# Kernel tuning notes

Hardware: AMD Instinct MI355X
Metric: run time of the kernel (lower is better)

Reference implementation:

```python
import jax, jax.numpy as jnp
import numpy as np

B, DIM, H, W = 8, 512, 32, 32
HC, WC = 32, 32
NH, DH = 8, 64
DE = NH * DH  # dim_embed = 512


def setup_inputs() -> dict:
    key = jax.random.key(0)
    ks = jax.random.split(key, 6)
    return {
        "x": jax.random.normal(ks[0], (B, DIM, H, W), jnp.float32),
        "context": jax.random.normal(ks[1], (B, DIM, HC, WC), jnp.float32),
        "gamma": jnp.ones((DIM, 1, 1), jnp.float32),
        "w_q": jax.random.normal(ks[2], (DE, DIM), jnp.float32) * 0.02,
        "w_k": jax.random.normal(ks[3], (DE, DIM), jnp.float32) * 0.02,
        "w_v": jax.random.normal(ks[4], (DE, DIM), jnp.float32) * 0.02,
        "w_proj": jax.random.normal(ks[5], (DIM, DE), jnp.float32) * 0.02,
    }


def _rms_norm(t, gamma, scale):
    # torch F.normalize(dim=1): x / max(||x||_2, 1e-12) along channel axis
    nrm = jnp.sqrt(jnp.sum(t * t, axis=1, keepdims=True))
    return t / jnp.maximum(nrm, 1e-12) * scale * gamma


def _split_heads(t, h, w):
    # 'b (c n) h w -> (b n) (h w) c' with c=DH, n=NH
    b = t.shape[0]
    t = t.reshape(b, DH, NH, h, w).transpose(0, 2, 3, 4, 1)  # b n h w c
    return t.reshape(b * NH, h * w, DH)


def reference(x, context, gamma, w_q, w_k, w_v, w_proj):
    scale = float(DIM) ** 0.5
    xn = _rms_norm(x, gamma, scale)
    # faithful to source bug: self.norm (not norm_context) applied to context
    cn = _rms_norm(context, gamma, scale)

    q = jnp.einsum('bchw,oc->bohw', xn, w_q)
    k = jnp.einsum('bchw,oc->bohw', cn, w_k)
    v = jnp.einsum('bchw,oc->bohw', cn, w_v)

    q = _split_heads(q, H, W)      # (B*NH, H*W, DH)
    k = _split_heads(k, HC, WC)    # (B*NH, HC*WC, DH)
    v = _split_heads(v, HC, WC)

    qk = jnp.einsum('bmc,bnc->bmn', q, k) * (float(DH) ** -0.5)
    attn = jnp.einsum('bmn,bnc->bmc', jax.nn.softmax(qk, axis=-1) + 1e-8, v) + 1e-8

    # '(b n) (h w) c -> b (c n) h w'
    attn = attn.reshape(B, NH, H, W, DH).transpose(0, 4, 1, 2, 3).reshape(B, DE, H, W)
    return jnp.einsum('bchw,oc->bohw', attn, w_proj)
```

## Files before the change

### kernel.cpp

```cpp
#include <hip/hip_runtime.h>
#include <hip/hip_bf16.h>


typedef _Float16 half8v __attribute__((ext_vector_type(8)));
typedef __attribute__((ext_vector_type(4))) float float4v;

__device__ inline ushort f2h(float f) {
  union { _Float16 h; ushort u; } cv;
  cv.h = (_Float16)f;
  return cv.u;
}

__device__ inline void stage16(const void* g, void* l) {
  __builtin_amdgcn_global_load_lds(
      (const __attribute__((address_space(1))) unsigned*)g,
      (__attribute__((address_space(3))) unsigned*)l, 16, 0, 0);
}

__global__ __launch_bounds__(256) void tq_kernel(
    const float* __restrict__ x, const float* __restrict__ ctx,
    ushort* __restrict__ xT, ushort* __restrict__ cT,
    float* __restrict__ sx, float* __restrict__ sc) {
  const int tensor = blockIdx.z;
  const int b = blockIdx.y;
  const int pos0 = blockIdx.x << 5;
  const float* src = tensor ? ctx : x;
  ushort* dstT = tensor ? cT : xT;
  float* dstS = tensor ? sc : sx;
  const int t = threadIdx.x;

  __shared__ ushort tile[32 * 512];
  __shared__ float part[32][32];
  unsigned* tile32 = (unsigned*)tile;

  const int pcq = t & 7;
  const int crg = t >> 3;
  float ssq[4] = {0.f, 0.f, 0.f, 0.f};

  const float* srcb = src + ((size_t)b * 512) * 1024 + pos0;
  for (int p = 0; p < 8; ++p) {
    const int cr0 = p * 64 + crg * 2;
    float4 v0 = *(const float4*)&srcb[(size_t)cr0 * 1024 + pcq * 4];
    float4 v1 = *(const float4*)&srcb[(size_t)(cr0 + 1) * 1024 + pcq * 4];
    ssq[0] += v0.x * v0.x + v1.x * v1.x;
    ssq[1] += v0.y * v0.y + v1.y * v1.y;
    ssq[2] += v0.z * v0.z + v1.z * v1.z;
    ssq[3] += v0.w * v0.w + v1.w * v1.w;
    const int cp = cr0 >> 1;
    float e0[4] = {v0.x, v0.y, v0.z, v0.w};
    float e1[4] = {v1.x, v1.y, v1.z, v1.w};
#pragma unroll
    for (int j = 0; j < 4; ++j) {
      const int posl = pcq * 4 + j;
      unsigned pk = (unsigned)f2h(e0[j]) | ((unsigned)f2h(e1[j]) << 16);
      tile32[posl * 256 + (cp ^ posl)] = pk;
    }
  }
#pragma unroll
  for (int j = 0; j < 4; ++j) part[crg][pcq * 4 + j] = ssq[j];
  __syncthreads();
  if (t < 32) {
    float s = 0.f;
#pragma unroll
    for (int g2 = 0; g2 < 32; ++g2) s += part[g2][t];
    dstS[b * 1024 + pos0 + t] = 22.627416997969522f / fmaxf(sqrtf(s), 1e-12f);
  }
  ushort* ob = dstT + ((size_t)b * 1024 + pos0) * 512;
#pragma unroll
  for (int ii = 0; ii < 8; ++ii) {
    const int m = t + ii * 256;
    const int posl = m >> 6, c16 = m & 63;
    uint4 u;
    u.x = tile32[posl * 256 + ((c16 * 4 + 0) ^ posl)];
    u.y = tile32[posl * 256 + ((c16 * 4 + 1) ^ posl)];
    u.z = tile32[posl * 256 + ((c16 * 4 + 2) ^ posl)];
    u.w = tile32[posl * 256 + ((c16 * 4 + 3) ^ posl)];
    *(uint4*)&ob[(size_t)posl * 512 + c16 * 8] = u;
  }
}

__global__ __launch_bounds__(256) void wconv_kernel(
    const float* __restrict__ wq, const float* __restrict__ wk,
    const float* __restrict__ wv, const float* __restrict__ wp,
    const float* __restrict__ gamma, ushort* __restrict__ wf) {
  const int m = blockIdx.y;
  const float* W = (m == 0) ? wq : (m == 1) ? wk : (m == 2) ? wv : wp;
  const int r = blockIdx.x * 4 + (threadIdx.x >> 6);
  const int c8 = (threadIdx.x & 63) * 8;
  ushort h[8];
  if (m < 3) {
    const int o = ((r & 63) << 3) + (r >> 6);
    const float* wr_ = &W[(size_t)o * 512 + c8];
#pragma unroll
    for (int j = 0; j < 8; ++j) h[j] = f2h(wr_[j] * gamma[c8 + j]);
  } else {
#pragma unroll
    for (int j = 0; j < 8; ++j) {
      const int cc = c8 + j;
      const int cs = ((cc & 63) << 3) + (cc >> 6);
      h[j] = f2h(W[(size_t)r * 512 + cs]);
    }
  }
  ushort* dst = &wf[((size_t)m * 512 + r) * 512 + c8];
  uint4 u;
  u.x = (unsigned)h[0] | ((unsigned)h[1] << 16);
  u.y = (unsigned)h[2] | ((unsigned)h[3] << 16);
  u.z = (unsigned)h[4] | ((unsigned)h[5] << 16);
  u.w = (unsigned)h[6] | ((unsigned)h[7] << 16);
  *(uint4*)dst = u;
}

__global__ __launch_bounds__(256, 2) void qkv_kernel(
    const ushort* __restrict__ xT, const ushort* __restrict__ cT,
    const ushort* __restrict__ wf, const float* __restrict__ sx,
    const float* __restrict__ sc, ushort* __restrict__ qh,
    ushort* __restrict__ kh, ushort* __restrict__ vt) {
  const int z = blockIdx.z;
  const int proj = z % 3;
  const int b = z / 3;
  const ushort* XT = (proj == 0) ? xT : cT;
  const float* S = (proj == 0) ? sx : sc;
  const ushort* WF = wf + (size_t)proj * 262144;
  const int pos0 = blockIdx.x << 7;
  const int o0 = blockIdx.y << 7;

  __shared__ __align__(16) unsigned char lds[65536];
  unsigned char* Al = lds;
  unsigned char* Bl = lds + 32768;

  const int t = threadIdx.x, w = t >> 6, lane = t & 63;
  const int g = lane >> 4, l15 = lane & 15;
  const int wr = w >> 1, wc = w & 1;
  const int srow_ = lane >> 3;
  const int sslot16 = ((lane & 7) ^ srow_) << 4;

  const unsigned char* Asrc =
      (const unsigned char*)(XT + ((size_t)b * 1024 + pos0) * 512);
  const unsigned char* Bsrc = (const unsigned char*)(WF + (size_t)o0 * 512);

#define QSTAGE(buf, kk)                                                     \
  do {                                                                      \
    _Pragma("unroll") for (int i = 0; i < 4; ++i) {                         \
      const int j = (w << 2) + i;                                           \
      stage16(Asrc + (size_t)((j << 3) + srow_) * 1024 + (kk)*128 + sslot16,\
              Al + (buf)*16384 + (j << 10));                                \
      stage16(Bsrc + (size_t)((j << 3) + srow_) * 1024 + (kk)*128 + sslot16,\
              Bl + (buf)*16384 + (j << 10));                                \
    }                                                                       \
  } while (0)

  float4v acc[4][4];
#pragma unroll
  for (int i = 0; i < 4; ++i)
#pragma unroll
    for (int j2 = 0; j2 < 4; ++j2) acc[i][j2] = (float4v){0.f, 0.f, 0.f, 0.f};

  QSTAGE(0, 0);
  __syncthreads();

  for (int kk = 0; kk < 8; ++kk) {
    const int cur = kk & 1;
    if (kk < 7) QSTAGE(cur ^ 1, kk + 1);
    const unsigned char* At = Al + cur * 16384;
    const unsigned char* Bt = Bl + cur * 16384;
    half8v af[4][2], bf[4][2];
#pragma unroll
    for (int mt = 0; mt < 4; ++mt) {
      const int row = (wr << 6) + (mt << 4) + l15;
      const unsigned char* rb = At + row * 128;
      af[mt][0] = *(const half8v*)(rb + (((g) ^ (row & 7)) << 4));
      af[mt][1] = *(const half8v*)(rb + (((4 + g) ^ (row & 7)) << 4));
    }
#pragma unroll
    for (int nt = 0; nt < 4; ++nt) {
      const int row = (wc << 6) + (nt << 4) + l15;
      const unsigned char* rb = Bt + row * 128;
      bf[nt][0] = *(const half8v*)(rb + (((g) ^ (row & 7)) << 4));
      bf[nt][1] = *(const half8v*)(rb + (((4 + g) ^ (row & 7)) << 4));
    }
    if (proj < 2) {
#pragma unroll
      for (int mt = 0; mt < 4; ++mt)
#pragma unroll
        for (int nt = 0; nt < 4; ++nt) {
          acc[mt][nt] = __builtin_amdgcn_mfma_f32_16x16x32_f16(
              af[mt][0], bf[nt][0], acc[mt][nt], 0, 0, 0);
          acc[mt][nt] = __builtin_amdgcn_mfma_f32_16x16x32_f16(
              af[mt][1], bf[nt][1], acc[mt][nt], 0, 0, 0);
        }
    } else {
#pragma unroll
      for (int mt = 0; mt < 4; ++mt)
#pragma unroll
        for (int nt = 0; nt < 4; ++nt) {
          acc[mt][nt] = __builtin_amdgcn_mfma_f32_16x16x32_f16(
              bf[nt][0], af[mt][0], acc[mt][nt], 0, 0, 0);
          acc[mt][nt] = __builtin_amdgcn_mfma_f32_16x16x32_f16(
              bf[nt][1], af[mt][1], acc[mt][nt], 0, 0, 0);
        }
    }
    __syncthreads();
  }
#undef QSTAGE

  if (proj < 2) {
    ushort* Out = (proj == 0) ? qh : kh;
#pragma unroll
    for (int mt = 0; mt < 4; ++mt) {
      const int posb = pos0 + (wr << 6) + (mt << 4) + (g << 2);
      float4 sv = *(const float4*)&S[b * 1024 + posb];
      float sarr[4] = {sv.x, sv.y, sv.z, sv.w};
#pragma unroll
      for (int nt = 0; nt < 4; ++nt) {
        const int oo = o0 + (wc << 6) + (nt << 4) + l15;
#pragma unroll
        for (int r = 0; r < 3 + 1; ++r) {
          float val = acc[mt][nt][r] * sarr[r];
          Out[((size_t)(b * 1024 + posb + r)) * 512 + oo] = f2h(val);
        }
      }
    }
  } else {
#pragma unroll
    for (int mt = 0; mt < 4; ++mt) {
      const int pos = pos0 + (wr << 6) + (mt << 4) + l15;
      const float sval = S[b * 1024 + pos];
#pragma unroll
      for (int nt = 0; nt < 4; ++nt) {
        const int ob = o0 + (wc << 6) + (nt << 4) + (g << 2);
#pragma unroll
        for (int r = 0; r < 4; ++r) {
          const int oo = ob + r;
          vt[((size_t)(b * 512 + oo)) * 1024 + pos] = f2h(acc[mt][nt][r] * sval);
        }
      }
    }
  }
}

__global__ __launch_bounds__(512, 2) void attn_kernel(
    const ushort* __restrict__ qh, const ushort* __restrict__ kh,
    const ushort* __restrict__ vt, ushort* __restrict__ am) {
  __shared__ __align__(16) unsigned char lds[65536];

  const int bh = blockIdx.y;
  const int b = bh >> 3, n = bh & 7;
  const int mbase = blockIdx.x << 8;
  const int t = threadIdx.x;
  const int w = t >> 6;
  const int lane = t & 63;
  const int g = lane >> 4;
  const int l15 = lane & 15;
  const int swz = (l15 & 7) << 4;

  half8v qf[2][2];
#pragma unroll
  for (int qt = 0; qt < 2; ++qt) {
    const size_t qrow = (size_t)b * 1024 + mbase + w * 32 + qt * 16 + l15;
#pragma unroll
    for (int c = 0; c < 2; ++c)
      qf[qt][c] = *(const half8v*)(qh + qrow * 512 + n * 64 + c * 32 + g * 8);
  }

  float4v o[2][4];
#pragma unroll
  for (int qt = 0; qt < 2; ++qt)
#pragma unroll
    for (int dt = 0; dt < 4; ++dt) o[qt][dt] = (float4v){0.f, 0.f, 0.f, 0.f};
  float rsum[2] = {0.f, 0.f};

  const int srow = (w << 3) + (lane >> 3);
  const int scol = ((lane & 7) ^ (lane >> 3)) << 4;
  const unsigned char* kgb =
      (const unsigned char*)(kh + (size_t)b * 524288 + n * 64) + srow * 1024 +
      scol;
  const unsigned char* vgb =
      (const unsigned char*)(vt + (size_t)(b * 8 + n) * 65536) + srow * 2048 +
      scol;
  unsigned char* Kl = lds;
  unsigned char* Vl = lds + 16384;
  unsigned char* Pl = lds + 32768 + w * 4096;

#define ASTAGE(buf, kt)                                            \
  do {                                                             \
    stage16(kgb + (size_t)(kt)*65536, Kl + (buf)*8192 + w * 1024); \
    stage16(vgb + (size_t)(kt)*128, Vl + (buf)*8192 + w * 1024);   \
  } while (0)

  ASTAGE(0, 0);
  __syncthreads();

  for (int kt = 0; kt < 16; ++kt) {
    const int cur = kt & 1;
    if (kt < 15) ASTAGE(cur ^ 1, kt + 1);

    const unsigned char* Kc = Kl + cur * 8192;
    const unsigned char* Vc = Vl + cur * 8192;

    float4v st[4][2];
#pragma unroll
    for (int ktile = 0; ktile < 4; ++ktile) {
      const unsigned char* krow = Kc + (ktile * 16 + l15) * 128;
      half8v kf0 = *(const half8v*)(krow + ((g * 16) ^ swz));
      half8v kf1 = *(const half8v*)(krow + ((64 + g * 16) ^ swz));
#pragma unroll
      for (int qt = 0; qt < 2; ++qt) {
        float4v a2 = {0.f, 0.f, 0.f, 0.f};
        a2 = __builtin_amdgcn_mfma_f32_16x16x32_f16(kf0, qf[qt][0], a2, 0, 0, 0);
        a2 = __builtin_amdgcn_mfma_f32_16x16x32_f16(kf1, qf[qt][1], a2, 0, 0, 0);
        st[ktile][qt] = a2;
      }
    }

#pragma unroll
    for (int qt = 0; qt < 2; ++qt) {
      unsigned char* prowp = Pl + (qt * 16 + l15) * 128;
#pragma unroll
      for (int ktile = 0; ktile < 4; ++ktile) {
        union { unsigned long long u; ushort s[4]; } pk;
        float4v sv = st[ktile][qt];
#pragma unroll
        for (int r = 0; r < 4; ++r) {
          float p = __expf(sv[r] * 0.125f);
          rsum[qt] += p;
          pk.s[r] = f2h(p);
        }
        *(unsigned long long*)(prowp + ((ktile * 32 + g * 8) ^ swz)) = pk.u;
      }
    }

    half8v pf[2][2];
#pragma unroll
    for (int qt = 0; qt < 2; ++qt)
#pragma unroll
      for (int c = 0; c < 2; ++c)
        pf[qt][c] = *(const half8v*)(Pl + (qt * 16 + l15) * 128 +
                                     ((c * 64 + g * 16) ^ swz));
#pragma unroll
    for (int dt = 0; dt < 4; ++dt) {
      const unsigned char* vrow = Vc + (dt * 16 + l15) * 128;
      half8v vf0 = *(const half8v*)(vrow + ((g * 16) ^ swz));
      half8v vf1 = *(const half8v*)(vrow + ((64 + g * 16) ^ swz));
#pragma unroll
      for (int qt = 0; qt < 2; ++qt) {
        o[qt][dt] = __builtin_amdgcn_mfma_f32_16x16x32_f16(pf[qt][0], vf0,
                                                           o[qt][dt], 0, 0, 0);
        o[qt][dt] = __builtin_amdgcn_mfma_f32_16x16x32_f16(pf[qt][1], vf1,
                                                           o[qt][dt], 0, 0, 0);
      }
    }
    __syncthreads();
  }
#undef ASTAGE

#pragma unroll
  for (int qt = 0; qt < 2; ++qt) {
    float r = rsum[qt];
    r += __shfl_xor(r, 16, 64);
    r += __shfl_xor(r, 32, 64);
    rsum[qt] = 1.0f / r;
  }

#pragma unroll
  for (int qt = 0; qt < 2; ++qt) {
#pragma unroll
    for (int dt = 0; dt < 4; ++dt) {
      float4v ov = o[qt][dt];
      const int d = dt * 16 + l15;
#pragma unroll
      for (int r = 0; r < 4; ++r) {
        float inv = __shfl(rsum[qt], (lane & 48) | (g * 4 + r), 64);
        const int pos = mbase + w * 32 + qt * 16 + g * 4 + r;
        am[((size_t)(b * 1024 + pos)) * 512 + n * 64 + d] = f2h(ov[r] * inv);
      }
    }
  }
}

__global__ __launch_bounds__(256, 2) void proj_kernel(
    const ushort* __restrict__ am, const ushort* __restrict__ wf3,
    float* __restrict__ out) {
  const int b = blockIdx.z;
  const int pos0 = blockIdx.x << 7;
  const int o0 = blockIdx.y << 7;

  __shared__ __align__(16) unsigned char lds[65536];
  unsigned char* Al = lds;
  unsigned char* Bl = lds + 32768;

  const int t = threadIdx.x, w = t >> 6, lane = t & 63;
  const int g = lane >> 4, l15 = lane & 15;
  const int wr = w >> 1, wc = w & 1;
  const int srow_ = lane >> 3;
  const int sslot16 = ((lane & 7) ^ srow_) << 4;

  const unsigned char* Asrc = (const unsigned char*)(wf3 + (size_t)o0 * 512);
  const unsigned char* Bsrc =
      (const unsigned char*)(am + ((size_t)b * 1024 + pos0) * 512);

#define PSTAGE(buf, kk)                                                     \
  do {                                                                      \
    _Pragma("unroll") for (int i = 0; i < 4; ++i) {                         \
      const int j = (w << 2) + i;                                           \
      stage16(Asrc + (size_t)((j << 3) + srow_) * 1024 + (kk)*128 + sslot16,\
              Al + (buf)*16384 + (j << 10));                                \
      stage16(Bsrc + (size_t)((j << 3) + srow_) * 1024 + (kk)*128 + sslot16,\
              Bl + (buf)*16384 + (j << 10));                                \
    }                                                                       \
  } while (0)

  float4v acc[4][4];
#pragma unroll
  for (int i = 0; i < 4; ++i)
#pragma unroll
    for (int j2 = 0; j2 < 4; ++j2) acc[i][j2] = (float4v){0.f, 0.f, 0.f, 0.f};

  PSTAGE(0, 0);
  __syncthreads();

  for (int kk = 0; kk < 8; ++kk) {
    const int cur = kk & 1;
    if (kk < 7) PSTAGE(cur ^ 1, kk + 1);
    const unsigned char* At = Al + cur * 16384;
    const unsigned char* Bt = Bl + cur * 16384;
    half8v af[4][2], bf[4][2];
#pragma unroll
    for (int mt = 0; mt < 4; ++mt) {
      const int row = (wr << 6) + (mt << 4) + l15;
      const unsigned char* rb = At + row * 128;
      af[mt][0] = *(const half8v*)(rb + (((g) ^ (row & 7)) << 4));
      af[mt][1] = *(const half8v*)(rb + (((4 + g) ^ (row & 7)) << 4));
    }
#pragma unroll
    for (int nt = 0; nt < 4; ++nt) {
      const int row = (wc << 6) + (nt << 4) + l15;
      const unsigned char* rb = Bt + row * 128;
      bf[nt][0] = *(const half8v*)(rb + (((g) ^ (row & 7)) << 4));
      bf[nt][1] = *(const half8v*)(rb + (((4 + g) ^ (row & 7)) << 4));
    }
#pragma unroll
    for (int mt = 0; mt < 4; ++mt)
#pragma unroll
      for (int nt = 0; nt < 4; ++nt) {
        acc[mt][nt] = __builtin_amdgcn_mfma_f32_16x16x32_f16(
            af[mt][0], bf[nt][0], acc[mt][nt], 0, 0, 0);
        acc[mt][nt] = __builtin_amdgcn_mfma_f32_16x16x32_f16(
            af[mt][1], bf[nt][1], acc[mt][nt], 0, 0, 0);
      }
    __syncthreads();
  }
#undef PSTAGE

#pragma unroll
  for (int mt = 0; mt < 4; ++mt) {
    const int ob = o0 + (wr << 6) + (mt << 4) + (g << 2);
#pragma unroll
    for (int nt = 0; nt < 4; ++nt) {
      const int pos = pos0 + (wc << 6) + (nt << 4) + l15;
#pragma unroll
      for (int r = 0; r < 4; ++r) {
        out[((size_t)(b * 512 + ob + r)) * 1024 + pos] = acc[mt][nt][r];
      }
    }
  }
}

extern "C" void kernel_launch(void* const* d_in, const int* in_sizes, int n_in,
                              void* d_out, int out_size, void* d_ws,
                              size_t ws_size, hipStream_t stream) {
  const float* x = (const float*)d_in[0];
  const float* ctx = (const float*)d_in[1];
  const float* gamma = (const float*)d_in[2];
  const float* wq = (const float*)d_in[3];
  const float* wk = (const float*)d_in[4];
  const float* wv = (const float*)d_in[5];
  const float* wp = (const float*)d_in[6];
  float* out = (float*)d_out;

  char* ws = (char*)d_ws;
  float* sx = (float*)(ws);
  float* sc = (float*)(ws + 32768);
  ushort* xT = (ushort*)(ws + 65536);
  ushort* cT = (ushort*)(ws + 65536 + 8388608);
  ushort* wf = (ushort*)(ws + 65536 + 16777216);
  ushort* qh = (ushort*)(ws + 65536 + 18874368);
  ushort* kh = (ushort*)(ws + 65536 + 27262976);
  ushort* vt = (ushort*)(ws + 65536 + 35651584);
  ushort* am = xT;

  tq_kernel<<<dim3(32, 8, 2), 256, 0, stream>>>(x, ctx, xT, cT, sx, sc);
  wconv_kernel<<<dim3(128, 4), 256, 0, stream>>>(wq, wk, wv, wp, gamma, wf);
  qkv_kernel<<<dim3(8, 4, 24), 256, 0, stream>>>(xT, cT, wf, sx, sc, qh, kh,
                                                 vt);
  attn_kernel<<<dim3(4, 64), 512, 0, stream>>>(qh, kh, vt, am);
  proj_kernel<<<dim3(8, 4, 8), 256, 0, stream>>>(am, wf + 3 * 262144, out);
}
```

Measured before the change: 68.69 us.

## Rewrite attention with 32x32x16 MFMA and register-resident P; merge prep kernels

The attention kernel moves from 16x16x32 MFMA tiles to 32x32x16 tiles, with 256 threads per block and 64 query rows per wave. The probability tile P now stays in registers and is rearranged with permlane32 swaps, so the LDS write/read round trip for P is gone. The 1/sqrt(d) scale is folded into the Q projection epilogue. The two preprocessing kernels are merged into one launch. In exchange, register pressure per wave rises and there are half as many waves per block.

```diff
diff --git a/kernel.cpp b/kernel.cpp
--- a/kernel.cpp
+++ b/kernel.cpp
@@ -3,7 +3,10 @@
 
 
 typedef _Float16 half8v __attribute__((ext_vector_type(8)));
+typedef __fp16 fp16x2 __attribute__((ext_vector_type(2)));
 typedef __attribute__((ext_vector_type(4))) float float4v;
+typedef __attribute__((ext_vector_type(16))) float float16v;
+typedef __attribute__((ext_vector_type(2))) int int2v;
 
 __device__ inline ushort f2h(float f) {
   union { _Float16 h; ushort u; } cv;
@@ -17,97 +20,116 @@
       (__attribute__((address_space(3))) unsigned*)l, 16, 0, 0);
 }
 
-__global__ __launch_bounds__(256) void tq_kernel(
+__device__ inline void permswap(unsigned& a, unsigned& b) {
+#if __has_builtin(__builtin_amdgcn_permlane32_swap)
+  int2v r = __builtin_amdgcn_permlane32_swap((int)a, (int)b, false, false);
+  a = (unsigned)r[0];
+  b = (unsigned)r[1];
+#else
+  unsigned pa = (unsigned)__shfl_xor((int)a, 32, 64);
+  unsigned pb = (unsigned)__shfl_xor((int)b, 32, 64);
+  bool hb = (threadIdx.x & 32) != 0;
+  unsigned na = hb ? pb : a;
+  unsigned nb = hb ? b : pa;
+  a = na;
+  b = nb;
+#endif
+}
+
+__global__ __launch_bounds__(256) void prep_kernel(
     const float* __restrict__ x, const float* __restrict__ ctx,
-    ushort* __restrict__ xT, ushort* __restrict__ cT,
-    float* __restrict__ sx, float* __restrict__ sc) {
-  const int tensor = blockIdx.z;
-  const int b = blockIdx.y;
-  const int pos0 = blockIdx.x << 5;
-  const float* src = tensor ? ctx : x;
-  ushort* dstT = tensor ? cT : xT;
-  float* dstS = tensor ? sc : sx;
-  const int t = threadIdx.x;
-
+    const float* __restrict__ wq, const float* __restrict__ wk,
+    const float* __restrict__ wv, const float* __restrict__ wp,
+    const float* __restrict__ gamma, ushort* __restrict__ xT,
+    ushort* __restrict__ cT, float* __restrict__ sx, float* __restrict__ sc,
+    ushort* __restrict__ wf) {
   __shared__ ushort tile[32 * 512];
   __shared__ float part[32][32];
-  unsigned* tile32 = (unsigned*)tile;
-
-  const int pcq = t & 7;
-  const int crg = t >> 3;
-  float ssq[4] = {0.f, 0.f, 0.f, 0.f};
-
-  const float* srcb = src + ((size_t)b * 512) * 1024 + pos0;
-  for (int p = 0; p < 8; ++p) {
-    const int cr0 = p * 64 + crg * 2;
-    float4 v0 = *(const float4*)&srcb[(size_t)cr0 * 1024 + pcq * 4];
-    float4 v1 = *(const float4*)&srcb[(size_t)(cr0 + 1) * 1024 + pcq * 4];
-    ssq[0] += v0.x * v0.x + v1.x * v1.x;
-    ssq[1] += v0.y * v0.y + v1.y * v1.y;
-    ssq[2] += v0.z * v0.z + v1.z * v1.z;
-    ssq[3] += v0.w * v0.w + v1.w * v1.w;
-    const int cp = cr0 >> 1;
-    float e0[4] = {v0.x, v0.y, v0.z, v0.w};
-    float e1[4] = {v1.x, v1.y, v1.z, v1.w};
-#pragma unroll
-    for (int j = 0; j < 4; ++j) {
-      const int posl = pcq * 4 + j;
-      unsigned pk = (unsigned)f2h(e0[j]) | ((unsigned)f2h(e1[j]) << 16);
-      tile32[posl * 256 + (cp ^ posl)] = pk;
-    }
-  }
-#pragma unroll
-  for (int j = 0; j < 4; ++j) part[crg][pcq * 4 + j] = ssq[j];
-  __syncthreads();
-  if (t < 32) {
-    float s = 0.f;
-#pragma unroll
-    for (int g2 = 0; g2 < 32; ++g2) s += part[g2][t];
-    dstS[b * 1024 + pos0 + t] = 22.627416997969522f / fmaxf(sqrtf(s), 1e-12f);
-  }
-  ushort* ob = dstT + ((size_t)b * 1024 + pos0) * 512;
-#pragma unroll
-  for (int ii = 0; ii < 8; ++ii) {
-    const int m = t + ii * 256;
-    const int posl = m >> 6, c16 = m & 63;
+  const int bid = blockIdx.x;
+  const int t = threadIdx.x;
+
+  if (bid < 512) {
+    const int tensor = bid >> 8;
+    const int b = (bid >> 5) & 7;
+    const int pos0 = (bid & 31) << 5;
+    const float* src = tensor ? ctx : x;
+    ushort* dstT = tensor ? cT : xT;
+    float* dstS = tensor ? sc : sx;
+    unsigned* tile32 = (unsigned*)tile;
+
+    const int pcq = t & 7;
+    const int crg = t >> 3;
+    float ssq[4] = {0.f, 0.f, 0.f, 0.f};
+
+    const float* srcb = src + ((size_t)b * 512) * 1024 + pos0;
+    for (int p = 0; p < 8; ++p) {
+      const int cr0 = p * 64 + crg * 2;
+      float4 v0 = *(const float4*)&srcb[(size_t)cr0 * 1024 + pcq * 4];
+      float4 v1 = *(const float4*)&srcb[(size_t)(cr0 + 1) * 1024 + pcq * 4];
+      ssq[0] += v0.x * v0.x + v1.x * v1.x;
+      ssq[1] += v0.y * v0.y + v1.y * v1.y;
+      ssq[2] += v0.z * v0.z + v1.z * v1.z;
+      ssq[3] += v0.w * v0.w + v1.w * v1.w;
+      const int cp = cr0 >> 1;
+      float e0[4] = {v0.x, v0.y, v0.z, v0.w};
+      float e1[4] = {v1.x, v1.y, v1.z, v1.w};
+#pragma unroll
+      for (int j = 0; j < 4; ++j) {
+        const int posl = pcq * 4 + j;
+        unsigned pk = (unsigned)f2h(e0[j]) | ((unsigned)f2h(e1[j]) << 16);
+        tile32[posl * 256 + (cp ^ posl)] = pk;
+      }
+    }
+#pragma unroll
+    for (int j = 0; j < 4; ++j) part[crg][pcq * 4 + j] = ssq[j];
+    __syncthreads();
+    if (t < 32) {
+      float s = 0.f;
+#pragma unroll
+      for (int g2 = 0; g2 < 32; ++g2) s += part[g2][t];
+      dstS[b * 1024 + pos0 + t] =
+          22.627416997969522f / fmaxf(sqrtf(s), 1e-12f);
+    }
+    ushort* ob = dstT + ((size_t)b * 1024 + pos0) * 512;
+#pragma unroll
+    for (int ii = 0; ii < 8; ++ii) {
+      const int m = t + ii * 256;
+      const int posl = m >> 6, c16 = m & 63;
+      uint4 u;
+      u.x = tile32[posl * 256 + ((c16 * 4 + 0) ^ posl)];
+      u.y = tile32[posl * 256 + ((c16 * 4 + 1) ^ posl)];
+      u.z = tile32[posl * 256 + ((c16 * 4 + 2) ^ posl)];
+      u.w = tile32[posl * 256 + ((c16 * 4 + 3) ^ posl)];
+      *(uint4*)&ob[(size_t)posl * 512 + c16 * 8] = u;
+    }
+  } else {
+    const int wbid = bid - 512;
+    const int m = wbid >> 7;
+    const float* W = (m == 0) ? wq : (m == 1) ? wk : (m == 2) ? wv : wp;
+    const int r = (wbid & 127) * 4 + (t >> 6);
+    const int c8 = (t & 63) * 8;
+    ushort h[8];
+    if (m < 3) {
+      const int o = ((r & 63) << 3) + (r >> 6);
+      const float* wr_ = &W[(size_t)o * 512 + c8];
+#pragma unroll
+      for (int j = 0; j < 8; ++j) h[j] = f2h(wr_[j] * gamma[c8 + j]);
+    } else {
+#pragma unroll
+      for (int j = 0; j < 8; ++j) {
+        const int cc = c8 + j;
+        const int cs = ((cc & 63) << 3) + (cc >> 6);
+        h[j] = f2h(W[(size_t)r * 512 + cs]);
+      }
+    }
+    ushort* dst = &wf[((size_t)m * 512 + r) * 512 + c8];
     uint4 u;
-    u.x = tile32[posl * 256 + ((c16 * 4 + 0) ^ posl)];
-    u.y = tile32[posl * 256 + ((c16 * 4 + 1) ^ posl)];
-    u.z = tile32[posl * 256 + ((c16 * 4 + 2) ^ posl)];
-    u.w = tile32[posl * 256 + ((c16 * 4 + 3) ^ posl)];
-    *(uint4*)&ob[(size_t)posl * 512 + c16 * 8] = u;
-  }
-}
-
-__global__ __launch_bounds__(256) void wconv_kernel(
-    const float* __restrict__ wq, const float* __restrict__ wk,
-    const float* __restrict__ wv, const float* __restrict__ wp,
-    const float* __restrict__ gamma, ushort* __restrict__ wf) {
-  const int m = blockIdx.y;
-  const float* W = (m == 0) ? wq : (m == 1) ? wk : (m == 2) ? wv : wp;
-  const int r = blockIdx.x * 4 + (threadIdx.x >> 6);
-  const int c8 = (threadIdx.x & 63) * 8;
-  ushort h[8];
-  if (m < 3) {
-    const int o = ((r & 63) << 3) + (r >> 6);
-    const float* wr_ = &W[(size_t)o * 512 + c8];
-#pragma unroll
-    for (int j = 0; j < 8; ++j) h[j] = f2h(wr_[j] * gamma[c8 + j]);
-  } else {
-#pragma unroll
-    for (int j = 0; j < 8; ++j) {
-      const int cc = c8 + j;
-      const int cs = ((cc & 63) << 3) + (cc >> 6);
-      h[j] = f2h(W[(size_t)r * 512 + cs]);
-    }
-  }
-  ushort* dst = &wf[((size_t)m * 512 + r) * 512 + c8];
-  uint4 u;
-  u.x = (unsigned)h[0] | ((unsigned)h[1] << 16);
-  u.y = (unsigned)h[2] | ((unsigned)h[3] << 16);
-  u.z = (unsigned)h[4] | ((unsigned)h[5] << 16);
-  u.w = (unsigned)h[6] | ((unsigned)h[7] << 16);
-  *(uint4*)dst = u;
+    u.x = (unsigned)h[0] | ((unsigned)h[1] << 16);
+    u.y = (unsigned)h[2] | ((unsigned)h[3] << 16);
+    u.z = (unsigned)h[4] | ((unsigned)h[5] << 16);
+    u.w = (unsigned)h[6] | ((unsigned)h[7] << 16);
+    *(uint4*)dst = u;
+  }
 }
 
 __global__ __launch_bounds__(256, 2) void qkv_kernel(
@@ -205,16 +227,17 @@
 
   if (proj < 2) {
     ushort* Out = (proj == 0) ? qh : kh;
+    const float qsc = (proj == 0) ? 0.125f : 1.0f;
 #pragma unroll
     for (int mt = 0; mt < 4; ++mt) {
       const int posb = pos0 + (wr << 6) + (mt << 4) + (g << 2);
-      float4 sv = *(const float4*)&S[b * 1024 + posb];
-      float sarr[4] = {sv.x, sv.y, sv.z, sv.w};
+      float4 sv4 = *(const float4*)&S[b * 1024 + posb];
+      float sarr[4] = {sv4.x * qsc, sv4.y * qsc, sv4.z * qsc, sv4.w * qsc};
 #pragma unroll
       for (int nt = 0; nt < 4; ++nt) {
         const int oo = o0 + (wc << 6) + (nt << 4) + l15;
 #pragma unroll
-        for (int r = 0; r < 3 + 1; ++r) {
+        for (int r = 0; r < 4; ++r) {
           float val = acc[mt][nt][r] * sarr[r];
           Out[((size_t)(b * 1024 + posb + r)) * 512 + oo] = f2h(val);
         }
@@ -238,10 +261,10 @@
   }
 }
 
-__global__ __launch_bounds__(512, 2) void attn_kernel(
+__global__ __launch_bounds__(256, 2) void attn_kernel(
     const ushort* __restrict__ qh, const ushort* __restrict__ kh,
     const ushort* __restrict__ vt, ushort* __restrict__ am) {
-  __shared__ __align__(16) unsigned char lds[65536];
+  __shared__ __align__(16) unsigned char lds[32768];
 
   const int bh = blockIdx.y;
   const int b = bh >> 3, n = bh & 7;
@@ -249,42 +272,47 @@
   const int t = threadIdx.x;
   const int w = t >> 6;
   const int lane = t & 63;
-  const int g = lane >> 4;
-  const int l15 = lane & 15;
-  const int swz = (l15 & 7) << 4;
-
-  half8v qf[2][2];
-#pragma unroll
-  for (int qt = 0; qt < 2; ++qt) {
-    const size_t qrow = (size_t)b * 1024 + mbase + w * 32 + qt * 16 + l15;
-#pragma unroll
-    for (int c = 0; c < 2; ++c)
-      qf[qt][c] = *(const half8v*)(qh + qrow * 512 + n * 64 + c * 32 + g * 8);
-  }
-
-  float4v o[2][4];
-#pragma unroll
-  for (int qt = 0; qt < 2; ++qt)
-#pragma unroll
-    for (int dt = 0; dt < 4; ++dt) o[qt][dt] = (float4v){0.f, 0.f, 0.f, 0.f};
+  const int l31 = lane & 31;
+  const int hi = lane >> 5;
+  const int swz = (l31 & 7) << 4;
+
+  half8v qf[2][4];
+#pragma unroll
+  for (int rowg = 0; rowg < 2; ++rowg) {
+    const size_t qrow = (size_t)b * 1024 + mbase + w * 64 + rowg * 32 + l31;
+#pragma unroll
+    for (int kc = 0; kc < 4; ++kc)
+      qf[rowg][kc] =
+          *(const half8v*)(qh + qrow * 512 + n * 64 + kc * 16 + hi * 8);
+  }
+
+  float16v o[2][2];
+#pragma unroll
+  for (int rowg = 0; rowg < 2; ++rowg)
+#pragma unroll
+    for (int d2 = 0; d2 < 2; ++d2)
+#pragma unroll
+      for (int e = 0; e < 16; ++e) o[rowg][d2][e] = 0.f;
   float rsum[2] = {0.f, 0.f};
 
-  const int srow = (w << 3) + (lane >> 3);
-  const int scol = ((lane & 7) ^ (lane >> 3)) << 4;
   const unsigned char* kgb =
-      (const unsigned char*)(kh + (size_t)b * 524288 + n * 64) + srow * 1024 +
-      scol;
+      (const unsigned char*)kh + (size_t)b * 1048576 + n * 128;
   const unsigned char* vgb =
-      (const unsigned char*)(vt + (size_t)(b * 8 + n) * 65536) + srow * 2048 +
-      scol;
-  unsigned char* Kl = lds;
-  unsigned char* Vl = lds + 16384;
-  unsigned char* Pl = lds + 32768 + w * 4096;
-
-#define ASTAGE(buf, kt)                                            \
-  do {                                                             \
-    stage16(kgb + (size_t)(kt)*65536, Kl + (buf)*8192 + w * 1024); \
-    stage16(vgb + (size_t)(kt)*128, Vl + (buf)*8192 + w * 1024);   \
+      (const unsigned char*)vt + (size_t)b * 1048576 + n * 131072;
+  const int u0 = t, u1 = t + 256;
+  const int kro0 = (u0 >> 3) * 1024 + ((((u0 & 7) ^ ((u0 >> 3) & 7))) << 4);
+  const int kro1 = (u1 >> 3) * 1024 + ((((u1 & 7) ^ ((u1 >> 3) & 7))) << 4);
+  const int vro0 = (u0 >> 3) * 2048 + ((((u0 & 7) ^ ((u0 >> 3) & 7))) << 4);
+  const int vro1 = (u1 >> 3) * 2048 + ((((u1 & 7) ^ ((u1 >> 3) & 7))) << 4);
+
+#define ASTAGE(buf, kt)                                                      \
+  do {                                                                       \
+    stage16(kgb + (size_t)(kt)*65536 + kro0, lds + (buf)*8192 + u0 * 16);    \
+    stage16(kgb + (size_t)(kt)*65536 + kro1, lds + (buf)*8192 + u1 * 16);    \
+    stage16(vgb + (size_t)(kt)*128 + vro0,                                   \
+            lds + 16384 + (buf)*8192 + u0 * 16);                             \
+    stage16(vgb + (size_t)(kt)*128 + vro1,                                   \
+            lds + 16384 + (buf)*8192 + u1 * 16);                             \
   } while (0)
 
   ASTAGE(0, 0);
@@ -293,85 +321,89 @@
   for (int kt = 0; kt < 16; ++kt) {
     const int cur = kt & 1;
     if (kt < 15) ASTAGE(cur ^ 1, kt + 1);
-
-    const unsigned char* Kc = Kl + cur * 8192;
-    const unsigned char* Vc = Vl + cur * 8192;
-
-    float4v st[4][2];
-#pragma unroll
-    for (int ktile = 0; ktile < 4; ++ktile) {
-      const unsigned char* krow = Kc + (ktile * 16 + l15) * 128;
-      half8v kf0 = *(const half8v*)(krow + ((g * 16) ^ swz));
-      half8v kf1 = *(const half8v*)(krow + ((64 + g * 16) ^ swz));
-#pragma unroll
-      for (int qt = 0; qt < 2; ++qt) {
-        float4v a2 = {0.f, 0.f, 0.f, 0.f};
-        a2 = __builtin_amdgcn_mfma_f32_16x16x32_f16(kf0, qf[qt][0], a2, 0, 0, 0);
-        a2 = __builtin_amdgcn_mfma_f32_16x16x32_f16(kf1, qf[qt][1], a2, 0, 0, 0);
-        st[ktile][qt] = a2;
-      }
-    }
-
-#pragma unroll
-    for (int qt = 0; qt < 2; ++qt) {
-      unsigned char* prowp = Pl + (qt * 16 + l15) * 128;
-#pragma unroll
-      for (int ktile = 0; ktile < 4; ++ktile) {
-        union { unsigned long long u; ushort s[4]; } pk;
-        float4v sv = st[ktile][qt];
-#pragma unroll
-        for (int r = 0; r < 4; ++r) {
-          float p = __expf(sv[r] * 0.125f);
-          rsum[qt] += p;
-          pk.s[r] = f2h(p);
+    const unsigned char* Kc = lds + cur * 8192;
+    const unsigned char* Vc = lds + 16384 + cur * 8192;
+
+    half8v vf[4][2];
+#pragma unroll
+    for (int ks = 0; ks < 4; ++ks)
+#pragma unroll
+      for (int d2 = 0; d2 < 2; ++d2)
+        vf[ks][d2] = *(const half8v*)(Vc + (l31 + 32 * d2) * 128 +
+                                      ((hi * 16 + ks * 32) ^ swz));
+
+#pragma unroll
+    for (int kt2 = 0; kt2 < 2; ++kt2) {
+      half8v kf[4];
+#pragma unroll
+      for (int kc = 0; kc < 4; ++kc)
+        kf[kc] = *(const half8v*)(Kc + (l31 + 32 * kt2) * 128 +
+                                  ((hi * 16 + kc * 32) ^ swz));
+#pragma unroll
+      for (int rowg = 0; rowg < 2; ++rowg) {
+        float16v st;
+#pragma unroll
+        for (int e = 0; e < 16; ++e) st[e] = 0.f;
+#pragma unroll
+        for (int kc = 0; kc < 4; ++kc)
+          st = __builtin_amdgcn_mfma_f32_32x32x16_f16(kf[kc], qf[rowg][kc],
+                                                      st, 0, 0, 0);
+        float p[16];
+#pragma unroll
+        for (int r = 0; r < 16; ++r) p[r] = __expf(st[r]);
+        rsum[rowg] += (((p[0] + p[1]) + (p[2] + p[3])) +
+                       ((p[4] + p[5]) + (p[6] + p[7]))) +
+                      (((p[8] + p[9]) + (p[10] + p[11])) +
+                       ((p[12] + p[13]) + (p[14] + p[15])));
+        unsigned wds[8];
+#pragma unroll
+        for (int j = 0; j < 8; ++j) {
+          union { fp16x2 h; unsigned u; } cv_;
+          cv_.h = __builtin_amdgcn_cvt_pkrtz(p[2 * j], p[2 * j + 1]);
+          wds[j] = cv_.u;
         }
-        *(unsigned long long*)(prowp + ((ktile * 32 + g * 8) ^ swz)) = pk.u;
-      }
-    }
-
-    half8v pf[2][2];
-#pragma unroll
-    for (int qt = 0; qt < 2; ++qt)
-#pragma unroll
-      for (int c = 0; c < 2; ++c)
-        pf[qt][c] = *(const half8v*)(Pl + (qt * 16 + l15) * 128 +
-                                     ((c * 64 + g * 16) ^ swz));
-#pragma unroll
-    for (int dt = 0; dt < 4; ++dt) {
-      const unsigned char* vrow = Vc + (dt * 16 + l15) * 128;
-      half8v vf0 = *(const half8v*)(vrow + ((g * 16) ^ swz));
-      half8v vf1 = *(const half8v*)(vrow + ((64 + g * 16) ^ swz));
-#pragma unroll
-      for (int qt = 0; qt < 2; ++qt) {
-        o[qt][dt] = __builtin_amdgcn_mfma_f32_16x16x32_f16(pf[qt][0], vf0,
-                                                           o[qt][dt], 0, 0, 0);
-        o[qt][dt] = __builtin_amdgcn_mfma_f32_16x16x32_f16(pf[qt][1], vf1,
-                                                           o[qt][dt], 0, 0, 0);
+        permswap(wds[0], wds[2]);
+        permswap(wds[1], wds[3]);
+        permswap(wds[4], wds[6]);
+        permswap(wds[5], wds[7]);
+        union { half8v h; unsigned u[4]; } pf0, pf1;
+        pf0.u[0] = wds[0]; pf0.u[1] = wds[1];
+        pf0.u[2] = wds[2]; pf0.u[3] = wds[3];
+        pf1.u[0] = wds[4]; pf1.u[1] = wds[5];
+        pf1.u[2] = wds[6]; pf1.u[3] = wds[7];
+#pragma unroll
+        for (int d2 = 0; d2 < 2; ++d2) {
+          o[rowg][d2] = __builtin_amdgcn_mfma_f32_32x32x16_f16(
+              pf0.h, vf[kt2 * 2 + 0][d2], o[rowg][d2], 0, 0, 0);
+          o[rowg][d2] = __builtin_amdgcn_mfma_f32_32x32x16_f16(
+              pf1.h, vf[kt2 * 2 + 1][d2], o[rowg][d2], 0, 0, 0);
+        }
       }
     }
     __syncthreads();
   }
 #undef ASTAGE
 
-#pragma unroll
-  for (int qt = 0; qt < 2; ++qt) {
-    float r = rsum[qt];
-    r += __shfl_xor(r, 16, 64);
-    r += __shfl_xor(r, 32, 64);
-    rsum[qt] = 1.0f / r;
-  }
-
-#pragma unroll
-  for (int qt = 0; qt < 2; ++qt) {
-#pragma unroll
-    for (int dt = 0; dt < 4; ++dt) {
-      float4v ov = o[qt][dt];
-      const int d = dt * 16 + l15;
-#pragma unroll
-      for (int r = 0; r < 4; ++r) {
-        float inv = __shfl(rsum[qt], (lane & 48) | (g * 4 + r), 64);
-        const int pos = mbase + w * 32 + qt * 16 + g * 4 + r;
-        am[((size_t)(b * 1024 + pos)) * 512 + n * 64 + d] = f2h(ov[r] * inv);
+  float inv[2];
+#pragma unroll
+  for (int rowg = 0; rowg < 2; ++rowg) {
+    float r = rsum[rowg] + __shfl_xor(rsum[rowg], 32, 64);
+    inv[rowg] = 1.0f / r;
+  }
+
+#pragma unroll
+  for (int rowg = 0; rowg < 2; ++rowg) {
+#pragma unroll
+    for (int r = 0; r < 16; ++r) {
+      const int qloc = (r & 3) + 8 * (r >> 2) + 4 * hi;
+      const float iv =
+          __shfl(inv[rowg], (r & 3) + 8 * (r >> 2) + ((lane >> 5) << 2), 64);
+      const size_t rowbase =
+          ((size_t)(b * 1024 + mbase + w * 64 + rowg * 32 + qloc)) * 512 +
+          n * 64 + l31;
+#pragma unroll
+      for (int d2 = 0; d2 < 2; ++d2) {
+        am[rowbase + 32 * d2] = f2h(o[rowg][d2][r] * iv);
       }
     }
   }
@@ -488,10 +520,10 @@
   ushort* vt = (ushort*)(ws + 65536 + 35651584);
   ushort* am = xT;
 
-  tq_kernel<<<dim3(32, 8, 2), 256, 0, stream>>>(x, ctx, xT, cT, sx, sc);
-  wconv_kernel<<<dim3(128, 4), 256, 0, stream>>>(wq, wk, wv, wp, gamma, wf);
+  prep_kernel<<<1024, 256, 0, stream>>>(x, ctx, wq, wk, wv, wp, gamma, xT, cT,
+                                        sx, sc, wf);
   qkv_kernel<<<dim3(8, 4, 24), 256, 0, stream>>>(xT, cT, wf, sx, sc, qh, kh,
                                                  vt);
-  attn_kernel<<<dim3(4, 64), 512, 0, stream>>>(qh, kh, vt, am);
+  attn_kernel<<<dim3(4, 64), 256, 0, stream>>>(qh, kh, vt, am);
   proj_kernel<<<dim3(8, 4, 8), 256, 0, stream>>>(am, wf + 3 * 262144, out);
 }
```

Measured after the change: 64.59 us. 1.06x faster.
